# Optimization experiments

Measured on AMD Instinct MI355X. Metric: run time of the kernel, lower is better.

Reference implementation:

```python
import jax, jax.numpy as jnp
import numpy as np

H = 512  # hidden_size

def setup_inputs() -> dict:
    key = jax.random.key(0)
    ks = jax.random.split(key, 5)
    B, S = 2, 512
    feats = jax.random.normal(ks[0], (B, S, H), dtype=jnp.float32)
    # torch Linear init ~ U(-1/sqrt(in), 1/sqrt(in)); scaled normals are fine for a reference
    W1 = jax.random.normal(ks[1], (2 * H, H), dtype=jnp.float32) / np.sqrt(2 * H)
    b1 = jnp.zeros((H,), dtype=jnp.float32)
    W2 = jax.random.normal(ks[2], (H, H // 2), dtype=jnp.float32) / np.sqrt(H)
    b2 = jnp.zeros((H // 2,), dtype=jnp.float32)
    W3 = jax.random.normal(ks[3], (H // 2, 1), dtype=jnp.float32) / np.sqrt(H // 2)
    b3 = jnp.zeros((1,), dtype=jnp.float32)
    return {"features": feats, "W1": W1, "b1": b1, "W2": W2, "b2": b2, "W3": W3, "b3": b3}


def reference(features, W1, b1, W2, b2, W3, b3):
    # cat([f_i, f_j]) @ W1 == f_i @ W1[:H] + f_j @ W1[H:]
    # Precompute the two halves once per residue instead of per pair.
    a = jnp.einsum('bsh,hk->bsk', features, W1[:H])          # [B,S,H]
    c = jnp.einsum('bsh,hk->bsk', features, W1[H:])          # [B,S,H]
    h1 = jax.nn.relu(a[:, :, None, :] + c[:, None, :, :] + b1)  # [B,S,S,H]
    # Dropout(0.1) is identity at inference.
    h2 = jax.nn.relu(jnp.einsum('bijh,hk->bijk', h1, W2) + b2)  # [B,S,S,H//2]
    logits = jnp.einsum('bijk,ko->bijo', h2, W3) + b3            # [B,S,S,1]
    return jax.nn.sigmoid(logits[..., 0])                        # [B,S,S]
```

## Files before the change

kernel.cpp:

```cpp
#include <hip/hip_runtime.h>

#define S_DIM 512
#define H_DIM 512
#define NH 256
#define TI 8
#define TJ 8

#define AS1 __attribute__((address_space(1)))
#define AS3 __attribute__((address_space(3)))

typedef _Float16 half8 __attribute__((ext_vector_type(8)));
typedef _Float16 half4 __attribute__((ext_vector_type(4)));
typedef float f32x4 __attribute__((ext_vector_type(4)));

__device__ __forceinline__ int swz(int r) { return ((r & 1) << 2) | (r >> 1); }

__global__ __launch_bounds__(256) void convert_all_kernel(const float* __restrict__ feats,
        const float* __restrict__ W1, const float* __restrict__ W2,
        _Float16* __restrict__ f16, _Float16* __restrict__ w1L, _Float16* __restrict__ w2L) {
    int blk = blockIdx.x;
    if (blk < 512) {
        int t = blk * 256 + threadIdx.x;
        float4 v = ((const float4*)feats)[t];
        half4 h;
        h.x = (_Float16)v.x; h.y = (_Float16)v.y; h.z = (_Float16)v.z; h.w = (_Float16)v.w;
        ((half4*)f16)[t] = h;
    } else if (blk < 768) {
        int t = (blk - 512) * 256 + threadIdx.x;
        int gcb = t >> 10, n = t & 1023;
        const float* src = (n < H_DIM) ? &W1[(size_t)(gcb * 8) * H_DIM + n]
                                       : &W1[(size_t)(H_DIM + gcb * 8) * H_DIM + (n - H_DIM)];
        half8 v;
#pragma unroll
        for (int j = 0; j < 8; j++) v[j] = (_Float16)src[(size_t)j * H_DIM];
        *(half8*)&w1L[((size_t)gcb * 1024 + n) * 8] = v;
    } else {
        int t = (blk - 768) * 256 + threadIdx.x;
        int gcb = t >> 8, n = t & 255;
        half8 v;
#pragma unroll
        for (int j = 0; j < 8; j++) v[j] = (_Float16)W2[(size_t)(gcb * 8 + j) * NH + n];
        *(half8*)&w2L[((size_t)gcb * 256 + n) * 8] = v;
    }
}

__global__ __launch_bounds__(256) void prep_mfma_kernel(const _Float16* __restrict__ f16,
        const _Float16* __restrict__ w1L, const float* __restrict__ b1,
        _Float16* __restrict__ aH, _Float16* __restrict__ cH) {
    const int n0 = blockIdx.x * 64, m0 = blockIdx.y * 64;
    const int tid = threadIdx.x, wave = tid >> 6, lane = tid & 63;
    const int quad = lane >> 4, l16 = lane & 15;
    const int wm = wave >> 1, wn = wave & 1;
    int mrow[2], ncol[2];
#pragma unroll
    for (int mt = 0; mt < 2; mt++) mrow[mt] = m0 + wm * 32 + mt * 16 + l16;
#pragma unroll
    for (int nt = 0; nt < 2; nt++) ncol[nt] = n0 + wn * 32 + nt * 16 + l16;
    f32x4 acc[2][2];
#pragma unroll
    for (int mt = 0; mt < 2; mt++)
#pragma unroll
        for (int nt = 0; nt < 2; nt++) acc[mt][nt] = (f32x4)0.f;
#pragma unroll
    for (int ks = 0; ks < 16; ks++) {
        int gcb = ks * 4 + quad;
        half8 af[2], bf[2];
#pragma unroll
        for (int mt = 0; mt < 2; mt++)
            af[mt] = *(const half8*)&f16[(size_t)mrow[mt] * H_DIM + gcb * 8];
#pragma unroll
        for (int nt = 0; nt < 2; nt++)
            bf[nt] = *(const half8*)&w1L[((size_t)gcb * 1024 + ncol[nt]) * 8];
#pragma unroll
        for (int nt = 0; nt < 2; nt++)
#pragma unroll
            for (int mt = 0; mt < 2; mt++)
                acc[mt][nt] = __builtin_amdgcn_mfma_f32_16x16x32_f16(af[mt], bf[nt],
                                                                     acc[mt][nt], 0, 0, 0);
    }
    const bool first_half = (n0 < H_DIM);
#pragma unroll
    for (int nt = 0; nt < 2; nt++) {
        float bias = first_half ? b1[ncol[nt]] : 0.f;
#pragma unroll
        for (int mt = 0; mt < 2; mt++)
#pragma unroll
            for (int r = 0; r < 4; r++) {
                int m = m0 + wm * 32 + mt * 16 + quad * 4 + r;
                float v = acc[mt][nt][r] + bias;
                if (first_half) aH[(size_t)m * H_DIM + ncol[nt]] = (_Float16)v;
                else            cH[(size_t)m * H_DIM + (ncol[nt] - H_DIM)] = (_Float16)v;
            }
    }
}

__global__ __launch_bounds__(256, 4) void pair_kernel(
        const _Float16* __restrict__ aH, const _Float16* __restrict__ cH,
        const _Float16* __restrict__ w2L,
        const float* __restrict__ b2, const float* __restrict__ W3,
        const float* __restrict__ b3, float* __restrict__ out) {
    const int jt = blockIdx.x, it = blockIdx.y, b = blockIdx.z;
    const int i0 = it * TI, j0 = jt * TJ;

    __shared__ __align__(16) _Float16 sa[TI * H_DIM];
    __shared__ __align__(16) _Float16 sc[TJ * H_DIM];
    __shared__ float spart[4][64];

    const int tid = threadIdx.x;
    const int wave = tid >> 6, lane = tid & 63;
    const int quad = lane >> 4, l16 = lane & 15;
    const int wn = wave;
    const int nb = wn * 64;

#pragma unroll
    for (int rr0 = 0; rr0 < 2; rr0++) {
        int rr = rr0 * 4 + wave;
        int gc = lane ^ swz(rr & 7);
        __builtin_amdgcn_global_load_lds(
            (const AS1 unsigned int*)&aH[((size_t)(b * S_DIM + i0 + rr)) * H_DIM + gc * 8],
            (AS3 unsigned int*)&sa[rr * H_DIM], 16, 0, 0);
        __builtin_amdgcn_global_load_lds(
            (const AS1 unsigned int*)&cH[((size_t)(b * S_DIM + j0 + rr)) * H_DIM + gc * 8],
            (AS3 unsigned int*)&sc[rr * H_DIM], 16, 0, 0);
    }

    int saoff[4], swzA[4];
#pragma unroll
    for (int mt = 0; mt < 4; mt++) {
        int il = (mt * 16 + l16) >> 3;
        saoff[mt] = il * H_DIM;
        swzA[mt] = swz(il);
    }
    const int jl = l16 & 7;
    const int scoff = jl * H_DIM, swzC = swz(jl);

    f32x4 acc[4][4];
#pragma unroll
    for (int mt = 0; mt < 4; mt++)
#pragma unroll
        for (int nt = 0; nt < 4; nt++) acc[mt][nt] = (f32x4)0.f;

    const _Float16* bp = &w2L[((size_t)quad * 256 + nb + l16) * 8];

    half8 bnxt[4];
#pragma unroll
    for (int nt = 0; nt < 4; nt++) bnxt[nt] = *(const half8*)&bp[nt * 16 * 8];

    __syncthreads();

#pragma unroll
    for (int ks = 0; ks < 16; ks++) {
        half8 bf[4];
#pragma unroll
        for (int nt = 0; nt < 4; nt++) bf[nt] = bnxt[nt];
        if (ks < 15) {
            const _Float16* bn = bp + (size_t)4 * 256 * 8;
#pragma unroll
            for (int nt = 0; nt < 4; nt++) bnxt[nt] = *(const half8*)&bn[nt * 16 * 8];
            bp = bn;
        }
        const int gcb = ks * 4 + quad;
        half8 vc = *(const half8*)&sc[scoff + (gcb ^ swzC) * 8];
        half8 af[4];
#pragma unroll
        for (int mt = 0; mt < 4; mt++) {
            half8 va = *(const half8*)&sa[saoff[mt] + (gcb ^ swzA[mt]) * 8];
            af[mt] = __builtin_elementwise_max(va + vc, (half8)(_Float16)0.f);
        }
#pragma unroll
        for (int nt = 0; nt < 4; nt++)
#pragma unroll
            for (int mt = 0; mt < 4; mt++)
                acc[mt][nt] = __builtin_amdgcn_mfma_f32_16x16x32_f16(af[mt], bf[nt],
                                                                     acc[mt][nt], 0, 0, 0);
    }

    float b2v[4], w3v[4];
#pragma unroll
    for (int nt = 0; nt < 4; nt++) {
        int n = nb + nt * 16 + l16;
        b2v[nt] = b2[n];
        w3v[nt] = W3[n];
    }
    float ps[4][4];
#pragma unroll
    for (int mt = 0; mt < 4; mt++)
#pragma unroll
        for (int r = 0; r < 4; r++) {
            float s = 0.f;
#pragma unroll
            for (int nt = 0; nt < 4; nt++) {
                float v = acc[mt][nt][r] + b2v[nt];
                v = v > 0.f ? v : 0.f;
                s += v * w3v[nt];
            }
            ps[mt][r] = s;
        }
#pragma unroll
    for (int mt = 0; mt < 4; mt++)
#pragma unroll
        for (int r = 0; r < 4; r++) {
            float s = ps[mt][r];
            s += __shfl_xor(s, 8, 16);
            s += __shfl_xor(s, 4, 16);
            s += __shfl_xor(s, 2, 16);
            s += __shfl_xor(s, 1, 16);
            ps[mt][r] = s;
        }
    if (l16 == 0) {
#pragma unroll
        for (int mt = 0; mt < 4; mt++)
#pragma unroll
            for (int r = 0; r < 4; r++)
                spart[wn][mt * 16 + quad * 4 + r] = ps[mt][r];
    }
    __syncthreads();
    if (tid < 64) {
        float tot = spart[0][tid] + spart[1][tid] + spart[2][tid] + spart[3][tid] + b3[0];
        float sg = 1.f / (1.f + __expf(-tot));
        int i = i0 + (tid >> 3), j = j0 + (tid & 7);
        out[(size_t)b * S_DIM * S_DIM + (size_t)i * S_DIM + j] = sg;
    }
}

extern "C" void kernel_launch(void* const* d_in, const int* in_sizes, int n_in,
                              void* d_out, int out_size, void* d_ws, size_t ws_size,
                              hipStream_t stream) {
    const float* feats = (const float*)d_in[0];
    const float* W1 = (const float*)d_in[1];
    const float* b1 = (const float*)d_in[2];
    const float* W2 = (const float*)d_in[3];
    const float* b2 = (const float*)d_in[4];
    const float* W3 = (const float*)d_in[5];
    const float* b3 = (const float*)d_in[6];
    float* out = (float*)d_out;

    const int B = in_sizes[0] / (S_DIM * H_DIM);
    const int M = B * S_DIM;

    char* ws = (char*)d_ws;
    _Float16* f16  = (_Float16*)ws;
    _Float16* aH   = (_Float16*)(ws + (1 << 20));
    _Float16* cH   = (_Float16*)(ws + (2 << 20));
    _Float16* w1L  = (_Float16*)(ws + (3 << 20));
    _Float16* w2L  = (_Float16*)(ws + (4 << 20));

    convert_all_kernel<<<832, 256, 0, stream>>>(feats, W1, W2, f16, w1L, w2L);
    prep_mfma_kernel<<<dim3(16, M / 64), 256, 0, stream>>>(f16, w1L, b1, aH, cH);
    pair_kernel<<<dim3(S_DIM / TJ, S_DIM / TI, B), 256, 0, stream>>>(aH, cH, w2L, b2, W3, b3, out);
}
```

Before: 210.1 us.

## Double pair-kernel row tile to 16 and reuse W2 fragments across more MFMAs

Raises TI from 8 to 16, so each block covers 16x8 residue pairs with 8 M-tiles of accumulators instead of 4. Each W2 fragment loaded from global memory now feeds twice as many MFMAs, cutting W2 traffic per pair in half. The cH row vector is also reused across more rows. The A-tile swizzle indexing is recomputed for the new layout and the epilogue is restructured per M-tile. Launch bounds drop to 2 blocks per CU because of the larger accumulator register footprint, which lowers occupancy and latency hiding.

```diff
diff --git a/kernel.cpp b/kernel.cpp
--- a/kernel.cpp
+++ b/kernel.cpp
@@ -3,7 +3,7 @@
 #define S_DIM 512
 #define H_DIM 512
 #define NH 256
-#define TI 8
+#define TI 16
 #define TJ 8
 
 #define AS1 __attribute__((address_space(1)))
@@ -94,7 +94,7 @@
     }
 }
 
-__global__ __launch_bounds__(256, 4) void pair_kernel(
+__global__ __launch_bounds__(256, 2) void pair_kernel(
         const _Float16* __restrict__ aH, const _Float16* __restrict__ cH,
         const _Float16* __restrict__ w2L,
         const float* __restrict__ b2, const float* __restrict__ W3,
@@ -104,7 +104,7 @@
 
     __shared__ __align__(16) _Float16 sa[TI * H_DIM];
     __shared__ __align__(16) _Float16 sc[TJ * H_DIM];
-    __shared__ float spart[4][64];
+    __shared__ float spart[4][TI * TJ];
 
     const int tid = threadIdx.x;
     const int wave = tid >> 6, lane = tid & 63;
@@ -113,30 +113,31 @@
     const int nb = wn * 64;
 
 #pragma unroll
-    for (int rr0 = 0; rr0 < 2; rr0++) {
+    for (int rr0 = 0; rr0 < 4; rr0++) {
         int rr = rr0 * 4 + wave;
         int gc = lane ^ swz(rr & 7);
         __builtin_amdgcn_global_load_lds(
             (const AS1 unsigned int*)&aH[((size_t)(b * S_DIM + i0 + rr)) * H_DIM + gc * 8],
             (AS3 unsigned int*)&sa[rr * H_DIM], 16, 0, 0);
+    }
+#pragma unroll
+    for (int rr0 = 0; rr0 < 2; rr0++) {
+        int rr = rr0 * 4 + wave;
+        int gc = lane ^ swz(rr);
         __builtin_amdgcn_global_load_lds(
             (const AS1 unsigned int*)&cH[((size_t)(b * S_DIM + j0 + rr)) * H_DIM + gc * 8],
             (AS3 unsigned int*)&sc[rr * H_DIM], 16, 0, 0);
     }
 
-    int saoff[4], swzA[4];
-#pragma unroll
-    for (int mt = 0; mt < 4; mt++) {
-        int il = (mt * 16 + l16) >> 3;
-        saoff[mt] = il * H_DIM;
-        swzA[mt] = swz(il);
-    }
+    const int hl = l16 >> 3;
+    const int abase = hl * H_DIM;
+    const int s0 = hl << 2;
     const int jl = l16 & 7;
     const int scoff = jl * H_DIM, swzC = swz(jl);
 
-    f32x4 acc[4][4];
-#pragma unroll
-    for (int mt = 0; mt < 4; mt++)
+    f32x4 acc[8][4];
+#pragma unroll
+    for (int mt = 0; mt < 8; mt++)
 #pragma unroll
         for (int nt = 0; nt < 4; nt++) acc[mt][nt] = (f32x4)0.f;
 
@@ -160,19 +161,16 @@
             bp = bn;
         }
         const int gcb = ks * 4 + quad;
-        half8 vc = *(const half8*)&sc[scoff + (gcb ^ swzC) * 8];
-        half8 af[4];
-#pragma unroll
-        for (int mt = 0; mt < 4; mt++) {
-            half8 va = *(const half8*)&sa[saoff[mt] + (gcb ^ swzA[mt]) * 8];
-            af[mt] = __builtin_elementwise_max(va + vc, (half8)(_Float16)0.f);
-        }
-#pragma unroll
-        for (int nt = 0; nt < 4; nt++)
-#pragma unroll
-            for (int mt = 0; mt < 4; mt++)
-                acc[mt][nt] = __builtin_amdgcn_mfma_f32_16x16x32_f16(af[mt], bf[nt],
+        half8 vc = *(const half8*)&sc[scoff + ((gcb ^ swzC) * 8)];
+#pragma unroll
+        for (int mt = 0; mt < 8; mt++) {
+            half8 va = *(const half8*)&sa[mt * 2 * H_DIM + abase + (((gcb ^ (mt & 3)) ^ s0) * 8)];
+            half8 afm = __builtin_elementwise_max(va + vc, (half8)(_Float16)0.f);
+#pragma unroll
+            for (int nt = 0; nt < 4; nt++)
+                acc[mt][nt] = __builtin_amdgcn_mfma_f32_16x16x32_f16(afm, bf[nt],
                                                                      acc[mt][nt], 0, 0, 0);
+        }
     }
 
     float b2v[4], w3v[4];
@@ -182,9 +180,9 @@
         b2v[nt] = b2[n];
         w3v[nt] = W3[n];
     }
-    float ps[4][4];
-#pragma unroll
-    for (int mt = 0; mt < 4; mt++)
+#pragma unroll
+    for (int mt = 0; mt < 8; mt++) {
+        float ps[4];
 #pragma unroll
         for (int r = 0; r < 4; r++) {
             float s = 0.f;
@@ -194,28 +192,20 @@
                 v = v > 0.f ? v : 0.f;
                 s += v * w3v[nt];
             }
-            ps[mt][r] = s;
-        }
-#pragma unroll
-    for (int mt = 0; mt < 4; mt++)
-#pragma unroll
-        for (int r = 0; r < 4; r++) {
-            float s = ps[mt][r];
             s += __shfl_xor(s, 8, 16);
             s += __shfl_xor(s, 4, 16);
             s += __shfl_xor(s, 2, 16);
             s += __shfl_xor(s, 1, 16);
-            ps[mt][r] = s;
-        }
-    if (l16 == 0) {
-#pragma unroll
-        for (int mt = 0; mt < 4; mt++)
+            ps[r] = s;
+        }
+        if (l16 == 0) {
 #pragma unroll
             for (int r = 0; r < 4; r++)
-                spart[wn][mt * 16 + quad * 4 + r] = ps[mt][r];
+                spart[wn][mt * 16 + quad * 4 + r] = ps[r];
+        }
     }
     __syncthreads();
-    if (tid < 64) {
+    if (tid < TI * TJ) {
         float tot = spart[0][tid] + spart[1][tid] + spart[2][tid] + spart[3][tid] + b3[0];
         float sg = 1.f / (1.f + __expf(-tot));
         int i = i0 + (tid >> 3), j = j0 + (tid & 7);
```

Result: faster. 202.6 us (-3.6%).

## Share relu(a+c) A-fragments across waves via double-buffered LDS

Applied to the files above, without the earlier changes.

Each wave used to recompute all four relu(a+c) A-fragments per k-step, so the same work was repeated by all four waves. Now each wave computes one fragment, stores it to a double-buffered LDS tile, and every wave reads all four back. This cuts redundant vector adds and LDS reads of sa/sc by four. The cost is 8 KB of extra shared memory and a workgroup barrier every k-step, which may stall the MFMA pipeline and lower occupancy.

```diff
diff --git a/kernel.cpp b/kernel.cpp
--- a/kernel.cpp
+++ b/kernel.cpp
@@ -104,13 +104,13 @@
 
     __shared__ __align__(16) _Float16 sa[TI * H_DIM];
     __shared__ __align__(16) _Float16 sc[TJ * H_DIM];
+    __shared__ __align__(16) _Float16 afb[2][4][512];
     __shared__ float spart[4][64];
 
     const int tid = threadIdx.x;
     const int wave = tid >> 6, lane = tid & 63;
     const int quad = lane >> 4, l16 = lane & 15;
-    const int wn = wave;
-    const int nb = wn * 64;
+    const int nb = wave * 64;
 
 #pragma unroll
     for (int rr0 = 0; rr0 < 2; rr0++) {
@@ -124,13 +124,10 @@
             (AS3 unsigned int*)&sc[rr * H_DIM], 16, 0, 0);
     }
 
-    int saoff[4], swzA[4];
-#pragma unroll
-    for (int mt = 0; mt < 4; mt++) {
-        int il = (mt * 16 + l16) >> 3;
-        saoff[mt] = il * H_DIM;
-        swzA[mt] = swz(il);
-    }
+    const int hl = l16 >> 3;
+    const int ilW = wave * 2 + hl;
+    const int saoffW = ilW * H_DIM;
+    const int swzAW = swz(ilW);
     const int jl = l16 & 7;
     const int scoff = jl * H_DIM, swzC = swz(jl);
 
@@ -148,8 +145,20 @@
 
     __syncthreads();
 
+    {
+        const int gcb = quad;
+        half8 va = *(const half8*)&sa[saoffW + ((gcb ^ swzAW) * 8)];
+        half8 vc = *(const half8*)&sc[scoff + ((gcb ^ swzC) * 8)];
+        half8 af = __builtin_elementwise_max(va + vc, (half8)(_Float16)0.f);
+        *(half8*)&afb[0][wave][lane * 8] = af;
+    }
+    asm volatile("s_waitcnt lgkmcnt(0)" ::: "memory");
+    __builtin_amdgcn_s_barrier();
+    __builtin_amdgcn_sched_barrier(0);
+
 #pragma unroll
     for (int ks = 0; ks < 16; ks++) {
+        const int buf = ks & 1;
         half8 bf[4];
 #pragma unroll
         for (int nt = 0; nt < 4; nt++) bf[nt] = bnxt[nt];
@@ -158,21 +167,27 @@
 #pragma unroll
             for (int nt = 0; nt < 4; nt++) bnxt[nt] = *(const half8*)&bn[nt * 16 * 8];
             bp = bn;
-        }
-        const int gcb = ks * 4 + quad;
-        half8 vc = *(const half8*)&sc[scoff + (gcb ^ swzC) * 8];
-        half8 af[4];
-#pragma unroll
-        for (int mt = 0; mt < 4; mt++) {
-            half8 va = *(const half8*)&sa[saoff[mt] + (gcb ^ swzA[mt]) * 8];
-            af[mt] = __builtin_elementwise_max(va + vc, (half8)(_Float16)0.f);
-        }
+            const int gcb = (ks + 1) * 4 + quad;
+            half8 va = *(const half8*)&sa[saoffW + ((gcb ^ swzAW) * 8)];
+            half8 vc = *(const half8*)&sc[scoff + ((gcb ^ swzC) * 8)];
+            half8 af = __builtin_elementwise_max(va + vc, (half8)(_Float16)0.f);
+            *(half8*)&afb[buf ^ 1][wave][lane * 8] = af;
+        }
+        half8 afr[4];
+#pragma unroll
+        for (int mt = 0; mt < 4; mt++)
+            afr[mt] = *(const half8*)&afb[buf][mt][lane * 8];
 #pragma unroll
         for (int nt = 0; nt < 4; nt++)
 #pragma unroll
             for (int mt = 0; mt < 4; mt++)
-                acc[mt][nt] = __builtin_amdgcn_mfma_f32_16x16x32_f16(af[mt], bf[nt],
+                acc[mt][nt] = __builtin_amdgcn_mfma_f32_16x16x32_f16(afr[mt], bf[nt],
                                                                      acc[mt][nt], 0, 0, 0);
+        if (ks < 15) {
+            asm volatile("s_waitcnt lgkmcnt(0)" ::: "memory");
+            __builtin_amdgcn_s_barrier();
+            __builtin_amdgcn_sched_barrier(0);
+        }
     }
 
     float b2v[4], w3v[4];
@@ -212,7 +227,7 @@
         for (int mt = 0; mt < 4; mt++)
 #pragma unroll
             for (int r = 0; r < 4; r++)
-                spart[wn][mt * 16 + quad * 4 + r] = ps[mt][r];
+                spart[wave][mt * 16 + quad * 4 + r] = ps[mt][r];
     }
     __syncthreads();
     if (tid < 64) {
```

After: 201.2 us. -4.2%, faster.
